# Kernel optimization log

Hardware: AMD Instinct MI355X
Metric: run time of the kernel (lower is better)

The kernel has to match this reference:

```python
import jax, jax.numpy as jnp
import numpy as np

N = 100000   # nodes
E = 1600000  # edges (avg degree 16)
IN = 128
HID = 128


def _glorot(key, shape):
    fan_in = shape[1]
    return jax.random.normal(key, shape, jnp.float32) * (1.0 / np.sqrt(fan_in))


def setup_inputs() -> dict:
    key = jax.random.key(0)
    ks = jax.random.split(key, 8)
    x = jax.random.normal(ks[0], (N, IN), jnp.float32)
    edge_index = jax.random.randint(ks[1], (2, E), 0, N, dtype=jnp.int64)
    return {
        "x": x,
        "edge_index": edge_index,
        "W1_l": _glorot(ks[2], (HID, IN)),
        "W1_r": _glorot(ks[3], (HID, IN)),
        "b1": jnp.zeros((HID,), jnp.float32),
        "W2_l": _glorot(ks[4], (HID, HID)),
        "W2_r": _glorot(ks[5], (HID, HID)),
        "b2": jnp.zeros((HID,), jnp.float32),
    }


def _sage_conv(x, src, dst, W_l, W_r, b):
    # message = x[src]; mean-aggregate onto dst; out = lin_l(mean) + lin_r(x) + b
    msg = x[src]                                                # [E, d]
    agg = jax.ops.segment_sum(msg, dst, num_segments=N)         # [N, d]
    cnt = jax.ops.segment_sum(jnp.ones((src.shape[0], 1), x.dtype), dst,
                              num_segments=N)                   # [N, 1]
    mean = agg / jnp.maximum(cnt, 1.0)
    return mean @ W_l.T + x @ W_r.T + b


def reference(x, edge_index, W1_l, W1_r, b1, W2_l, W2_r, b2):
    src, dst = edge_index[0], edge_index[1]
    h = jax.nn.relu(_sage_conv(x, src, dst, W1_l, W1_r, b1))
    return _sage_conv(h, src, dst, W2_l, W2_r, b2)
```

## Files before the change

kernel.cpp:

```cpp
#include <hip/hip_runtime.h>
#include <stdint.h>

#define N_NODES 100000
#define NE      1600000
#define DIM     128
#define NBUCKET 391

typedef __attribute__((ext_vector_type(8)))  __bf16 bf16x8;
typedef __attribute__((ext_vector_type(16))) float  f32x16;

#define ROW_B   0u
#define BHIST_B 401408u
#define BBASE_B 403456u
#define BCUR_B  405504u
#define SRC_B   409600u
#define XB_B    6809600u
#define HB_B    32409600u
#define MB_B    58009600u
#define W1_B    83609600u
#define W2_B    83675136u
#define BPAIR_B 83740672u

__device__ __forceinline__ uint32_t f2b_rne(float f) {
    uint32_t u = __float_as_uint(f);
    return (u + 0x7FFFu + ((u >> 16) & 1u)) >> 16;
}
__device__ __forceinline__ float b2f_lo(uint32_t u) { return __uint_as_float(u << 16); }
__device__ __forceinline__ float b2f_hi(uint32_t u) { return __uint_as_float(u & 0xFFFF0000u); }

#define BK_WG   512
#define BK_EPW  3125

__global__ __launch_bounds__(1024) void k_bhist(const int* __restrict__ dst,
                                                int* __restrict__ bhist) {
    __shared__ int h[392];
    const int tid = threadIdx.x;
    if (tid < 392) h[tid] = 0;
    __syncthreads();
    const int e0 = blockIdx.x * BK_EPW;
    const int e1 = e0 + BK_EPW;
    for (int e = e0 + tid; e < e1; e += 1024)
        atomicAdd(&h[dst[e] >> 8], 1);
    __syncthreads();
    if (tid < 392) {
        int v = h[tid];
        if (v) atomicAdd(&bhist[tid], v);
    }
}

__global__ __launch_bounds__(512) void k_bscan(const int* __restrict__ bhist,
                                               int* __restrict__ bbase,
                                               int* __restrict__ bcur) {
    __shared__ int sm[512];
    const int tid = threadIdx.x;
    int v = (tid < NBUCKET) ? bhist[tid] : 0;
    sm[tid] = v;
    __syncthreads();
    for (int off = 1; off < 512; off <<= 1) {
        int t = (tid >= off) ? sm[tid - off] : 0;
        __syncthreads();
        sm[tid] += t;
        __syncthreads();
    }
    int ex = sm[tid] - v;
    if (tid <= NBUCKET) bbase[tid] = ex;
    if (tid < NBUCKET) bcur[tid] = ex;
}

__global__ __launch_bounds__(1024) void k_bucket(
    const int* __restrict__ src, const int* __restrict__ dst,
    int* __restrict__ bcur, int2* __restrict__ bpair) {
    __shared__ int hist[392];
    __shared__ int base[392];
    __shared__ int cur[392];
    const int tid = threadIdx.x;
    const int e0 = blockIdx.x * BK_EPW;
    const int e1 = e0 + BK_EPW;

    if (tid < 392) { hist[tid] = 0; cur[tid] = 0; }
    __syncthreads();
    for (int e = e0 + tid; e < e1; e += 1024)
        atomicAdd(&hist[dst[e] >> 8], 1);
    __syncthreads();
    if (tid < 392) {
        int h = hist[tid];
        base[tid] = h ? atomicAdd(&bcur[tid], h) : 0;
    }
    __syncthreads();
    for (int e = e0 + tid; e < e1; e += 1024) {
        int d = dst[e];
        int b = d >> 8;
        int loc = atomicAdd(&cur[b], 1);
        bpair[(size_t)(base[b] + loc)] = make_int2(src[e], d);
    }
}

__global__ __launch_bounds__(256) void k_sortb(
    const int* __restrict__ bbase, const int2* __restrict__ bpair,
    int* __restrict__ rowptr, int* __restrict__ ssrc) {
    __shared__ int deg[256];
    __shared__ int sm[256];
    __shared__ int cur[256];
    const int b = blockIdx.x;
    const int tid = threadIdx.x;
    const int n0 = b << 8;
    const int bstart = bbase[b];
    const int bend   = bbase[b + 1];

    deg[tid] = 0;
    __syncthreads();
    for (int e = bstart + tid; e < bend; e += 256)
        atomicAdd(&deg[bpair[e].y & 255], 1);
    __syncthreads();
    int v = deg[tid];
    sm[tid] = v;
    __syncthreads();
    for (int off = 1; off < 256; off <<= 1) {
        int t = (tid >= off) ? sm[tid - off] : 0;
        __syncthreads();
        sm[tid] += t;
        __syncthreads();
    }
    int ex = sm[tid] - v;
    int idx = n0 + tid;
    if (idx <= N_NODES) rowptr[idx] = bstart + ex;
    cur[tid] = bstart + ex;
    __syncthreads();
    for (int e = bstart + tid; e < bend; e += 256) {
        int2 p = bpair[e];
        int slot = atomicAdd(&cur[p.y & 255], 1);
        ssrc[slot] = p.x;
    }
}

__global__ __launch_bounds__(256) void k_cvt_x(const float* __restrict__ x, uint32_t* __restrict__ xb) {
    size_t i = (size_t)blockIdx.x * 256 + threadIdx.x;
    if (i * 4 >= (size_t)N_NODES * DIM) return;
    float4 v = *reinterpret_cast<const float4*>(x + i * 4);
    uint2 o;
    o.x = f2b_rne(v.x) | (f2b_rne(v.y) << 16);
    o.y = f2b_rne(v.z) | (f2b_rne(v.w) << 16);
    *reinterpret_cast<uint2*>(xb + i * 2) = o;
}

__global__ __launch_bounds__(256) void k_cvt_w(
    const float* __restrict__ W1l, const float* __restrict__ W1r,
    const float* __restrict__ W2l, const float* __restrict__ W2r,
    uint16_t* __restrict__ w1, uint16_t* __restrict__ w2) {
    int gid = blockIdx.x * 256 + threadIdx.x;
    int layer = gid >> 13;
    int e = (gid & 8191) * 4;
    int row = e >> 8;
    int col = e & 255;
    const float* Wl = layer ? W2l : W1l;
    const float* Wr = layer ? W2r : W1r;
    const float* srcm = (col < 128) ? Wl : Wr;
    int c = col & 127;
    float4 v = *reinterpret_cast<const float4*>(&srcm[row * 128 + c]);
    uint2 o;
    o.x = f2b_rne(v.x) | (f2b_rne(v.y) << 16);
    o.y = f2b_rne(v.z) | (f2b_rne(v.w) << 16);
    uint16_t* wd = layer ? w2 : w1;
    *reinterpret_cast<uint2*>(&wd[row * 256 + col]) = o;
}

__global__ __launch_bounds__(256) void k_agg(const int* __restrict__ rowptr,
                                             const int* __restrict__ ssrc,
                                             const uint32_t* __restrict__ featb,
                                             uint32_t* __restrict__ meanb) {
    int node = (int)((blockIdx.x * 256 + threadIdx.x) >> 6);
    if (node >= N_NODES) return;
    int lane = threadIdx.x & 63;
    int start = rowptr[node];
    int end   = rowptr[node + 1];

    float ax0 = 0.f, ay0 = 0.f, ax1 = 0.f, ay1 = 0.f;
    float ax2 = 0.f, ay2 = 0.f, ax3 = 0.f, ay3 = 0.f;

    int e = start;
    for (; e + 8 <= end; e += 8) {
        int s0 = ssrc[e + 0], s1 = ssrc[e + 1], s2 = ssrc[e + 2], s3 = ssrc[e + 3];
        int s4 = ssrc[e + 4], s5 = ssrc[e + 5], s6 = ssrc[e + 6], s7 = ssrc[e + 7];
        uint32_t u0 = featb[(size_t)s0 * 64 + lane];
        uint32_t u1 = featb[(size_t)s1 * 64 + lane];
        uint32_t u2 = featb[(size_t)s2 * 64 + lane];
        uint32_t u3 = featb[(size_t)s3 * 64 + lane];
        uint32_t u4 = featb[(size_t)s4 * 64 + lane];
        uint32_t u5 = featb[(size_t)s5 * 64 + lane];
        uint32_t u6 = featb[(size_t)s6 * 64 + lane];
        uint32_t u7 = featb[(size_t)s7 * 64 + lane];
        ax0 += b2f_lo(u0); ay0 += b2f_hi(u0);
        ax1 += b2f_lo(u1); ay1 += b2f_hi(u1);
        ax2 += b2f_lo(u2); ay2 += b2f_hi(u2);
        ax3 += b2f_lo(u3); ay3 += b2f_hi(u3);
        ax0 += b2f_lo(u4); ay0 += b2f_hi(u4);
        ax1 += b2f_lo(u5); ay1 += b2f_hi(u5);
        ax2 += b2f_lo(u6); ay2 += b2f_hi(u6);
        ax3 += b2f_lo(u7); ay3 += b2f_hi(u7);
    }
    if (e + 4 <= end) {
        int s0 = ssrc[e + 0], s1 = ssrc[e + 1], s2 = ssrc[e + 2], s3 = ssrc[e + 3];
        uint32_t u0 = featb[(size_t)s0 * 64 + lane];
        uint32_t u1 = featb[(size_t)s1 * 64 + lane];
        uint32_t u2 = featb[(size_t)s2 * 64 + lane];
        uint32_t u3 = featb[(size_t)s3 * 64 + lane];
        ax0 += b2f_lo(u0); ay0 += b2f_hi(u0);
        ax1 += b2f_lo(u1); ay1 += b2f_hi(u1);
        ax2 += b2f_lo(u2); ay2 += b2f_hi(u2);
        ax3 += b2f_lo(u3); ay3 += b2f_hi(u3);
        e += 4;
    }
    for (; e < end; ++e) {
        int s = ssrc[e];
        uint32_t u = featb[(size_t)s * 64 + lane];
        ax0 += b2f_lo(u); ay0 += b2f_hi(u);
    }

    int cnt = end - start;
    float inv = cnt > 0 ? 1.0f / (float)cnt : 0.0f;
    float ax = ((ax0 + ax1) + (ax2 + ax3)) * inv;
    float ay = ((ay0 + ay1) + (ay2 + ay3)) * inv;
    meanb[(size_t)node * 64 + lane] = f2b_rne(ax) | (f2b_rne(ay) << 16);
}

template <bool RELU, bool BF16_OUT>
__global__ __launch_bounds__(256) void k_layer(
    const uint16_t* __restrict__ meanb, const uint16_t* __restrict__ xb,
    const uint16_t* __restrict__ wcat, const float* __restrict__ bias,
    void* __restrict__ outp)
{
    const int tid = threadIdx.x;
    const int lane = tid & 63;
    const int w = tid >> 6;
    const int wm = (w >> 1) * 64, wn = (w & 1) * 64;
    const int lrow = lane & 31, lk = (lane >> 5) * 8;
    const int base = blockIdx.x * 128;

    f32x16 acc00, acc01, acc10, acc11;
#pragma unroll
    for (int r = 0; r < 16; ++r) { acc00[r] = 0.f; acc01[r] = 0.f; acc10[r] = 0.f; acc11[r] = 0.f; }

    int r0 = base + wm + lrow;
    int r1 = r0 + 32;
    if (r0 > N_NODES - 1) r0 = N_NODES - 1;
    if (r1 > N_NODES - 1) r1 = N_NODES - 1;
    const uint16_t* a0m = meanb + (size_t)r0 * DIM + lk;
    const uint16_t* a1m = meanb + (size_t)r1 * DIM + lk;
    const uint16_t* a0x = xb   + (size_t)r0 * DIM + lk;
    const uint16_t* a1x = xb   + (size_t)r1 * DIM + lk;
    const uint16_t* b0p = wcat + (size_t)(wn + lrow) * 256 + lk;
    const uint16_t* b1p = wcat + (size_t)(wn + 32 + lrow) * 256 + lk;

#pragma unroll
    for (int ks = 0; ks < 16; ++ks) {
        const int klocal = (ks & 7) * 16;
        bf16x8 a0 = *reinterpret_cast<const bf16x8*>(((ks < 8) ? a0m : a0x) + klocal);
        bf16x8 a1 = *reinterpret_cast<const bf16x8*>(((ks < 8) ? a1m : a1x) + klocal);
        bf16x8 b0 = *reinterpret_cast<const bf16x8*>(b0p + ks * 16);
        bf16x8 b1 = *reinterpret_cast<const bf16x8*>(b1p + ks * 16);
        acc00 = __builtin_amdgcn_mfma_f32_32x32x16_bf16(a0, b0, acc00, 0, 0, 0);
        acc01 = __builtin_amdgcn_mfma_f32_32x32x16_bf16(a0, b1, acc01, 0, 0, 0);
        acc10 = __builtin_amdgcn_mfma_f32_32x32x16_bf16(a1, b0, acc10, 0, 0, 0);
        acc11 = __builtin_amdgcn_mfma_f32_32x32x16_bf16(a1, b1, acc11, 0, 0, 0);
    }

    const float bc0 = bias[wn + lrow];
    const float bc1 = bias[wn + 32 + lrow];
    const int hi4 = 4 * (lane >> 5);

#define STORE_TILE(ACC, MI, NI, BB)                                            \
    {                                                                          \
        const int colg = wn + (NI) * 32 + lrow;                                \
        _Pragma("unroll")                                                      \
        for (int r = 0; r < 16; ++r) {                                         \
            int rowg = base + wm + (MI) * 32 + (r & 3) + 8 * (r >> 2) + hi4;   \
            if (rowg < N_NODES) {                                              \
                float v = ACC[r] + (BB);                                       \
                if (RELU) v = fmaxf(v, 0.0f);                                  \
                if (BF16_OUT)                                                  \
                    ((uint16_t*)outp)[(size_t)rowg * DIM + colg] =             \
                        (uint16_t)f2b_rne(v);                                  \
                else                                                           \
                    ((float*)outp)[(size_t)rowg * DIM + colg] = v;             \
            }                                                                  \
        }                                                                      \
    }
    STORE_TILE(acc00, 0, 0, bc0)
    STORE_TILE(acc01, 0, 1, bc1)
    STORE_TILE(acc10, 1, 0, bc0)
    STORE_TILE(acc11, 1, 1, bc1)
#undef STORE_TILE
}

extern "C" void kernel_launch(void* const* d_in, const int* in_sizes, int n_in,
                              void* d_out, int out_size, void* d_ws, size_t ws_size,
                              hipStream_t stream) {
    const float* x   = (const float*)d_in[0];
    const int*   ei  = (const int*)d_in[1];
    const float* W1l = (const float*)d_in[2];
    const float* W1r = (const float*)d_in[3];
    const float* b1  = (const float*)d_in[4];
    const float* W2l = (const float*)d_in[5];
    const float* W2r = (const float*)d_in[6];
    const float* b2  = (const float*)d_in[7];
    const int* src = ei;
    const int* dst = ei + NE;

    char* wsb = (char*)d_ws;
    int*      rowptr  = (int*)(wsb + ROW_B);
    int*      bhist   = (int*)(wsb + BHIST_B);
    int*      bbase   = (int*)(wsb + BBASE_B);
    int*      bcur    = (int*)(wsb + BCUR_B);
    int*      ssrc    = (int*)(wsb + SRC_B);
    uint32_t* xb32    = (uint32_t*)(wsb + XB_B);
    uint16_t* xb16    = (uint16_t*)(wsb + XB_B);
    uint32_t* hb32    = (uint32_t*)(wsb + HB_B);
    uint16_t* hb16    = (uint16_t*)(wsb + HB_B);
    uint32_t* mb32    = (uint32_t*)(wsb + MB_B);
    uint16_t* mb16    = (uint16_t*)(wsb + MB_B);
    uint16_t* w1      = (uint16_t*)(wsb + W1_B);
    uint16_t* w2      = (uint16_t*)(wsb + W2_B);
    int2*     bpair   = (int2*)(wsb + BPAIR_B);
    float*    outf    = (float*)d_out;

    hipMemsetAsync(bhist, 0, 392 * sizeof(int), stream);

    k_bhist <<<BK_WG, 1024, 0, stream>>>(dst, bhist);
    k_bscan <<<1, 512, 0, stream>>>(bhist, bbase, bcur);
    k_bucket<<<BK_WG, 1024, 0, stream>>>(src, dst, bcur, bpair);
    k_sortb <<<NBUCKET, 256, 0, stream>>>(bbase, bpair, rowptr, ssrc);

    k_cvt_x<<<12500, 256, 0, stream>>>(x, xb32);
    k_cvt_w<<<64, 256, 0, stream>>>(W1l, W1r, W2l, W2r, w1, w2);

    const int agg_blocks = N_NODES / 4;
    const int layer_blocks = (N_NODES + 127) / 128;

    k_agg<<<agg_blocks, 256, 0, stream>>>(rowptr, ssrc, xb32, mb32);
    k_layer<true, true><<<layer_blocks, 256, 0, stream>>>(mb16, xb16, w1, b1, (void*)hb16);

    k_agg<<<agg_blocks, 256, 0, stream>>>(rowptr, ssrc, hb32, mb32);
    k_layer<false, false><<<layer_blocks, 256, 0, stream>>>(mb16, hb16, w2, b2, (void*)outf);
}
```

Baseline: 380.3 us.

## Pack bucket pairs, unroll aggregation by 16, stage weights in LDS

Bucket entries are packed into one 32-bit word (src<<8 | dst low byte) instead of an int2, halving the bucket-sort traffic. The aggregation loop gathers 16 neighbours per iteration so more loads are in flight. The layer GEMM stages the weight matrix in swizzled shared memory in two halves instead of each wave reading it from global memory. The costs are extra barriers, a 32KB LDS allocation per block that may lower occupancy, and more registers in the aggregation kernel.

```diff
diff --git a/kernel.cpp b/kernel.cpp
--- a/kernel.cpp
+++ b/kernel.cpp
@@ -69,7 +69,7 @@
 
 __global__ __launch_bounds__(1024) void k_bucket(
     const int* __restrict__ src, const int* __restrict__ dst,
-    int* __restrict__ bcur, int2* __restrict__ bpair) {
+    int* __restrict__ bcur, uint32_t* __restrict__ bpair) {
     __shared__ int hist[392];
     __shared__ int base[392];
     __shared__ int cur[392];
@@ -91,12 +91,12 @@
         int d = dst[e];
         int b = d >> 8;
         int loc = atomicAdd(&cur[b], 1);
-        bpair[(size_t)(base[b] + loc)] = make_int2(src[e], d);
+        bpair[(size_t)(base[b] + loc)] = ((uint32_t)src[e] << 8) | (uint32_t)(d & 255);
     }
 }
 
 __global__ __launch_bounds__(256) void k_sortb(
-    const int* __restrict__ bbase, const int2* __restrict__ bpair,
+    const int* __restrict__ bbase, const uint32_t* __restrict__ bpair,
     int* __restrict__ rowptr, int* __restrict__ ssrc) {
     __shared__ int deg[256];
     __shared__ int sm[256];
@@ -110,7 +110,7 @@
     deg[tid] = 0;
     __syncthreads();
     for (int e = bstart + tid; e < bend; e += 256)
-        atomicAdd(&deg[bpair[e].y & 255], 1);
+        atomicAdd(&deg[bpair[e] & 255u], 1);
     __syncthreads();
     int v = deg[tid];
     sm[tid] = v;
@@ -127,9 +127,9 @@
     cur[tid] = bstart + ex;
     __syncthreads();
     for (int e = bstart + tid; e < bend; e += 256) {
-        int2 p = bpair[e];
-        int slot = atomicAdd(&cur[p.y & 255], 1);
-        ssrc[slot] = p.x;
+        uint32_t p = bpair[e];
+        int slot = atomicAdd(&cur[p & 255u], 1);
+        ssrc[slot] = (int)(p >> 8);
     }
 }
 
@@ -178,7 +178,22 @@
     float ax2 = 0.f, ay2 = 0.f, ax3 = 0.f, ay3 = 0.f;
 
     int e = start;
-    for (; e + 8 <= end; e += 8) {
+    for (; e + 16 <= end; e += 16) {
+        int s[16];
+#pragma unroll
+        for (int j = 0; j < 16; ++j) s[j] = ssrc[e + j];
+        uint32_t u[16];
+#pragma unroll
+        for (int j = 0; j < 16; ++j) u[j] = featb[(size_t)s[j] * 64 + lane];
+#pragma unroll
+        for (int j = 0; j < 16; j += 4) {
+            ax0 += b2f_lo(u[j + 0]); ay0 += b2f_hi(u[j + 0]);
+            ax1 += b2f_lo(u[j + 1]); ay1 += b2f_hi(u[j + 1]);
+            ax2 += b2f_lo(u[j + 2]); ay2 += b2f_hi(u[j + 2]);
+            ax3 += b2f_lo(u[j + 3]); ay3 += b2f_hi(u[j + 3]);
+        }
+    }
+    if (e + 8 <= end) {
         int s0 = ssrc[e + 0], s1 = ssrc[e + 1], s2 = ssrc[e + 2], s3 = ssrc[e + 3];
         int s4 = ssrc[e + 4], s5 = ssrc[e + 5], s6 = ssrc[e + 6], s7 = ssrc[e + 7];
         uint32_t u0 = featb[(size_t)s0 * 64 + lane];
@@ -197,6 +212,7 @@
         ax1 += b2f_lo(u5); ay1 += b2f_hi(u5);
         ax2 += b2f_lo(u6); ay2 += b2f_hi(u6);
         ax3 += b2f_lo(u7); ay3 += b2f_hi(u7);
+        e += 8;
     }
     if (e + 4 <= end) {
         int s0 = ssrc[e + 0], s1 = ssrc[e + 1], s2 = ssrc[e + 2], s3 = ssrc[e + 3];
@@ -229,6 +245,8 @@
     const uint16_t* __restrict__ wcat, const float* __restrict__ bias,
     void* __restrict__ outp)
 {
+    __shared__ uint16_t Bs[128 * 128];
+
     const int tid = threadIdx.x;
     const int lane = tid & 63;
     const int w = tid >> 6;
@@ -248,16 +266,50 @@
     const uint16_t* a1m = meanb + (size_t)r1 * DIM + lk;
     const uint16_t* a0x = xb   + (size_t)r0 * DIM + lk;
     const uint16_t* a1x = xb   + (size_t)r1 * DIM + lk;
-    const uint16_t* b0p = wcat + (size_t)(wn + lrow) * 256 + lk;
-    const uint16_t* b1p = wcat + (size_t)(wn + 32 + lrow) * 256 + lk;
-
-#pragma unroll
-    for (int ks = 0; ks < 16; ++ks) {
-        const int klocal = (ks & 7) * 16;
-        bf16x8 a0 = *reinterpret_cast<const bf16x8*>(((ks < 8) ? a0m : a0x) + klocal);
-        bf16x8 a1 = *reinterpret_cast<const bf16x8*>(((ks < 8) ? a1m : a1x) + klocal);
-        bf16x8 b0 = *reinterpret_cast<const bf16x8*>(b0p + ks * 16);
-        bf16x8 b1 = *reinterpret_cast<const bf16x8*>(b1p + ks * 16);
+
+    const int srow = tid >> 1, shalf = tid & 1;
+    const int sx = (srow & 7) << 3;
+    const uint16_t* wsrc = wcat + srow * 256 + shalf * 64;
+    uint16_t* wdst = Bs + srow * 128;
+
+    const int rx = ((wn + lrow) & 7) << 3;
+    const uint16_t* bsp0 = Bs + (wn + lrow) * 128;
+    const uint16_t* bsp1 = Bs + (wn + 32 + lrow) * 128;
+
+#pragma unroll
+    for (int g = 0; g < 8; ++g) {
+        int c = shalf * 64 + g * 8;
+        *reinterpret_cast<uint4*>(wdst + (c ^ sx)) =
+            *reinterpret_cast<const uint4*>(wsrc + g * 8);
+    }
+    __syncthreads();
+#pragma unroll
+    for (int ks = 0; ks < 8; ++ks) {
+        const int klocal = ks * 16;
+        bf16x8 a0 = *reinterpret_cast<const bf16x8*>(a0m + klocal);
+        bf16x8 a1 = *reinterpret_cast<const bf16x8*>(a1m + klocal);
+        bf16x8 b0 = *reinterpret_cast<const bf16x8*>(bsp0 + ((klocal + lk) ^ rx));
+        bf16x8 b1 = *reinterpret_cast<const bf16x8*>(bsp1 + ((klocal + lk) ^ rx));
+        acc00 = __builtin_amdgcn_mfma_f32_32x32x16_bf16(a0, b0, acc00, 0, 0, 0);
+        acc01 = __builtin_amdgcn_mfma_f32_32x32x16_bf16(a0, b1, acc01, 0, 0, 0);
+        acc10 = __builtin_amdgcn_mfma_f32_32x32x16_bf16(a1, b0, acc10, 0, 0, 0);
+        acc11 = __builtin_amdgcn_mfma_f32_32x32x16_bf16(a1, b1, acc11, 0, 0, 0);
+    }
+    __syncthreads();
+#pragma unroll
+    for (int g = 0; g < 8; ++g) {
+        int c = shalf * 64 + g * 8;
+        *reinterpret_cast<uint4*>(wdst + (c ^ sx)) =
+            *reinterpret_cast<const uint4*>(wsrc + 128 + g * 8);
+    }
+    __syncthreads();
+#pragma unroll
+    for (int ks = 0; ks < 8; ++ks) {
+        const int klocal = ks * 16;
+        bf16x8 a0 = *reinterpret_cast<const bf16x8*>(a0x + klocal);
+        bf16x8 a1 = *reinterpret_cast<const bf16x8*>(a1x + klocal);
+        bf16x8 b0 = *reinterpret_cast<const bf16x8*>(bsp0 + ((klocal + lk) ^ rx));
+        bf16x8 b1 = *reinterpret_cast<const bf16x8*>(bsp1 + ((klocal + lk) ^ rx));
         acc00 = __builtin_amdgcn_mfma_f32_32x32x16_bf16(a0, b0, acc00, 0, 0, 0);
         acc01 = __builtin_amdgcn_mfma_f32_32x32x16_bf16(a0, b1, acc01, 0, 0, 0);
         acc10 = __builtin_amdgcn_mfma_f32_32x32x16_bf16(a1, b0, acc10, 0, 0, 0);
@@ -320,7 +372,7 @@
     uint16_t* mb16    = (uint16_t*)(wsb + MB_B);
     uint16_t* w1      = (uint16_t*)(wsb + W1_B);
     uint16_t* w2      = (uint16_t*)(wsb + W2_B);
-    int2*     bpair   = (int2*)(wsb + BPAIR_B);
+    uint32_t* bpair   = (uint32_t*)(wsb + BPAIR_B);
     float*    outf    = (float*)d_out;
 
     hipMemsetAsync(bhist, 0, 392 * sizeof(int), stream);
```

After: 368.3 us. 1.03x faster.
